# Kernel optimization log

Hardware: AMD Instinct MI355X
Metric: run time of the kernel (lower is better)

Reference implementation:

```python
import jax, jax.numpy as jnp
import numpy as np

N_HEADS = 16
D_EMBD = 1024
B, T = 2, 2048


def setup_inputs() -> dict:
    key = jax.random.key(0)
    k1, k2, k3 = jax.random.split(key, 3)
    x = jax.random.normal(k1, (B, T, D_EMBD), dtype=jnp.float32)
    W1 = jax.random.normal(k2, (D_EMBD, 3 * D_EMBD), dtype=jnp.float32) / np.sqrt(D_EMBD)
    b1 = jnp.zeros((3 * D_EMBD,), dtype=jnp.float32)
    W2 = jax.random.normal(k3, (D_EMBD, D_EMBD), dtype=jnp.float32) / np.sqrt(D_EMBD)
    b2 = jnp.zeros((D_EMBD,), dtype=jnp.float32)
    return {"x": x, "W1": W1, "b1": b1, "W2": W2, "b2": b2}


def reference(x, W1, b1, W2, b2):
    bs, t, d = x.shape
    h = N_HEADS
    kqv = x @ W1 + b1  # [b, t, 3d]
    # note original split order: k, q, v
    k, q, v = jnp.split(kqv, 3, axis=-1)
    # [b, t, d] -> [b, h, t, dh]
    def to_heads(z):
        return z.reshape(bs, t, h, d // h).transpose(0, 2, 1, 3)
    k, q, v = to_heads(k), to_heads(q), to_heads(v)
    mask = jnp.tril(jnp.ones((t, t), dtype=bool))
    attn = jnp.where(mask, jnp.einsum('bhqd,bhkd->bhqk', q, k), 0.0)  # softmax-free retention
    out = jnp.einsum('bhqk,bhkd->bhqd', attn, v)
    out = out.transpose(0, 2, 1, 3).reshape(bs, t, d)  # [b, t, d]
    return out @ W2 + b2
```

## Files before the change

kernel.cpp:

```cpp
#include <hip/hip_runtime.h>
#include <hip/hip_bf16.h>

typedef __bf16 bf16x8 __attribute__((ext_vector_type(8)));
typedef float f32x4 __attribute__((ext_vector_type(4)));
typedef float f32x16 __attribute__((ext_vector_type(16)));
typedef unsigned short ushort_t;
typedef unsigned short ushort8 __attribute__((ext_vector_type(8)));
typedef unsigned int uint4v __attribute__((ext_vector_type(4)));


__device__ inline void gload_lds16(const void* g, void* l) {
  __builtin_amdgcn_global_load_lds(
      (const __attribute__((address_space(1))) void*)g,
      (__attribute__((address_space(3))) void*)l, 16, 0, 0);
}

__device__ inline ushort_t f2bf(float f) {
  unsigned int u = __float_as_uint(f);
  unsigned int lsb = (u >> 16) & 1u;
  u += 0x7fffu + lsb;
  return (ushort_t)(u >> 16);
}


__global__ __launch_bounds__(256) void f32_to_bf16_vec(
    const float* __restrict__ in, ushort_t* __restrict__ out) {
  int i = (blockIdx.x * 256 + threadIdx.x) * 8;
  float4 a = *(const float4*)&in[i];
  float4 b = *(const float4*)&in[i + 4];
  ushort8 o;
  o[0] = f2bf(a.x); o[1] = f2bf(a.y); o[2] = f2bf(a.z); o[3] = f2bf(a.w);
  o[4] = f2bf(b.x); o[5] = f2bf(b.y); o[6] = f2bf(b.z); o[7] = f2bf(b.w);
  *(ushort8*)&out[i] = o;
}

__global__ __launch_bounds__(256) void transpose_f32_bf16(
    const float* __restrict__ in, ushort_t* __restrict__ out, int R, int C) {
  __shared__ float tile[32][33];
  const int tx = threadIdx.x & 31, ty = threadIdx.x >> 5;
  const int c0 = blockIdx.x * 32, r0 = blockIdx.y * 32;
#pragma unroll
  for (int i = 0; i < 32; i += 8)
    tile[ty + i][tx] = in[(size_t)(r0 + ty + i) * C + c0 + tx];
  __syncthreads();
#pragma unroll
  for (int i = 0; i < 32; i += 8)
    out[(size_t)(c0 + ty + i) * R + r0 + tx] = f2bf(tile[tx][ty + i]);
}

__global__ __launch_bounds__(256) void transpose_v(
    const ushort_t* __restrict__ kqv, ushort_t* __restrict__ vt) {
  __shared__ ushort_t tile[64 * 64];
  const int tt = blockIdx.x;
  const int bh = blockIdx.y;
  const int b = bh >> 4, h = bh & 15;
  const int tid = threadIdx.x;
#pragma unroll
  for (int p = 0; p < 2; p++) {
    const int tr = (tid >> 3) + p * 32;
    const int c8 = tid & 7;
    ushort8 v = *(const ushort8*)&kqv[(size_t)(b * 2048 + tt * 64 + tr) * 3072 +
                                      2048 + h * 64 + c8 * 8];
    *(ushort8*)&tile[tr * 64 + ((c8 ^ (tr & 7)) * 8)] = v;
  }
  __syncthreads();
  const int d = tid & 63;
#pragma unroll
  for (int p = 0; p < 2; p++) {
    const int t8 = (tid >> 6) + p * 4;
    ushort8 o;
#pragma unroll
    for (int j = 0; j < 8; j++) {
      const int t = t8 * 8 + j;
      o[j] = tile[t * 64 + (((d >> 3) ^ (t & 7)) * 8) + (d & 7)];
    }
    *(ushort8*)&vt[(size_t)(bh * 64 + d) * 2048 + tt * 64 + t8 * 8] = o;
  }
}


template <bool OUT_BF16>
__global__ __launch_bounds__(256) void gemm_bt(
    const ushort_t* __restrict__ A, const ushort_t* __restrict__ BT,
    const float* __restrict__ bias, void* __restrict__ Cout,
    int M, int N, int K) {
  __shared__ ushort_t lA[128 * 32];
  __shared__ ushort_t lB[128 * 32];
  const int tid = threadIdx.x;
  const int lane = tid & 63;
  const int wave = tid >> 6;
  const int wr = wave >> 1, wc = wave & 1;
  const int l16 = lane & 15, lhi = lane >> 4;
  const int bx = blockIdx.x, by = blockIdx.y;

  const ushort_t* gA = A + (size_t)(by * 128 + (tid >> 2)) * K + (tid & 3) * 8;
  const ushort_t* gB = BT + (size_t)(bx * 128 + (tid >> 2)) * K + (tid & 3) * 8;

  f32x4 acc[4][4] = {};

  for (int k0 = 0; k0 < K; k0 += 32) {
    gload_lds16(gA + k0, &lA[tid * 8]);
    gload_lds16(gA + k0 + (size_t)64 * K, &lA[tid * 8 + 2048]);
    gload_lds16(gB + k0, &lB[tid * 8]);
    gload_lds16(gB + k0 + (size_t)64 * K, &lB[tid * 8 + 2048]);
    __syncthreads();

    bf16x8 af[4], bfr[4];
#pragma unroll
    for (int m = 0; m < 4; m++)
      af[m] = *(const bf16x8*)&lA[(wr * 64 + m * 16 + l16) * 32 + lhi * 8];
#pragma unroll
    for (int n = 0; n < 4; n++)
      bfr[n] = *(const bf16x8*)&lB[(wc * 64 + n * 16 + l16) * 32 + lhi * 8];
#pragma unroll
    for (int m = 0; m < 4; m++)
#pragma unroll
      for (int n = 0; n < 4; n++)
        acc[m][n] = __builtin_amdgcn_mfma_f32_16x16x32_bf16(af[m], bfr[n],
                                                            acc[m][n], 0, 0, 0);
    __syncthreads();
  }

  const int r0 = by * 128 + wr * 64 + lhi * 4;
  const int c0 = bx * 128 + wc * 64 + l16;
#pragma unroll
  for (int m = 0; m < 4; m++)
#pragma unroll
    for (int n = 0; n < 4; n++) {
      const int col = c0 + n * 16;
      const float bv = bias[col];
#pragma unroll
      for (int j = 0; j < 4; j++) {
        const int row = r0 + m * 16 + j;
        const float v = acc[m][n][j] + bv;
        if (OUT_BF16)
          ((ushort_t*)Cout)[(size_t)row * N + col] = f2bf(v);
        else
          ((float*)Cout)[(size_t)row * N + col] = v;
      }
    }
}


__global__ __launch_bounds__(256) void attn_kernel(
    const ushort_t* __restrict__ kqv, const ushort_t* __restrict__ vt,
    ushort_t* __restrict__ ao) {
  __shared__ ushort_t lK[3][64 * 64];
  __shared__ ushort_t lVT[3][64 * 64];
  const int tid = threadIdx.x, lane = tid & 63, wave = tid >> 6;
  const int q_rel = lane & 31, hi = lane >> 5;
  const int L = blockIdx.x;
  const int W = (L & 7) * 64 + (L >> 3);
  const int qi = 15 - (W & 15);
  const int bh = W >> 4;
  const int b = bh >> 4, h = bh & 15;
  const int q0 = qi * 128;
  const ushort_t* base = kqv + (size_t)b * 2048 * 3072;
  const ushort_t* vbase = vt + (size_t)bh * 64 * 2048;

  size_t kg[2], vg[2];
  int ld[2];
#pragma unroll
  for (int p = 0; p < 2; p++) {
    const int slot = tid + p * 256;
    const int srow = slot >> 3;
    const int scb = (((slot & 7) * 16) ^ ((srow & 7) << 4)) >> 1;
    kg[p] = (size_t)srow * 3072 + h * 64 + scb;
    vg[p] = (size_t)srow * 2048 + scb;
    ld[p] = slot * 8;
  }

  const int wq0 = q0 + wave * 32;
  bf16x8 qf[4];
#pragma unroll
  for (int ds = 0; ds < 4; ds++)
    qf[ds] = *(const bf16x8*)&base[(size_t)(wq0 + q_rel) * 3072 + 1024 + h * 64 +
                                   ds * 16 + hi * 8];

  f32x16 oacc[2] = {};
  const int nkt = qi * 2 + 2;

#pragma unroll
  for (int p = 0; p < 2; p++) {
    gload_lds16(&base[kg[p]], &lK[0][ld[p]]);
    gload_lds16(&vbase[vg[p]], &lVT[0][ld[p]]);
  }
#pragma unroll
  for (int p = 0; p < 2; p++) {
    gload_lds16(&base[(size_t)64 * 3072 + kg[p]], &lK[1][ld[p]]);
    gload_lds16(&vbase[64 + vg[p]], &lVT[1][ld[p]]);
  }

  int cur = 0;
  for (int kt = 0; kt < nkt; ++kt) {
    if (kt + 1 < nkt) asm volatile("s_waitcnt vmcnt(4)" ::: "memory");
    else              asm volatile("s_waitcnt vmcnt(0)" ::: "memory");
    __builtin_amdgcn_s_barrier();
    asm volatile("" ::: "memory");

    if (kt + 2 < nkt) {
      const int pf = (cur + 2 >= 3) ? cur - 1 : cur + 2;
#pragma unroll
      for (int p = 0; p < 2; p++) {
        gload_lds16(&base[(size_t)(kt + 2) * 64 * 3072 + kg[p]], &lK[pf][ld[p]]);
        gload_lds16(&vbase[(size_t)(kt + 2) * 64 + vg[p]], &lVT[pf][ld[p]]);
      }
    }

    if (kt * 64 <= wq0 + 31) {
      const bool need_mask = (kt * 64 + 63) > wq0;
#pragma unroll
      for (int kb = 0; kb < 2; kb++) {
        f32x16 st = {};
        const int krow = kb * 32 + q_rel;
        const int ksw = krow & 7;
#pragma unroll
        for (int ds = 0; ds < 4; ds++) {
          bf16x8 kf = *(const bf16x8*)&lK[cur][krow * 64 + (((ds * 2 + hi) ^ ksw) * 8)];
          st = __builtin_amdgcn_mfma_f32_32x32x16_bf16(kf, qf[ds], st, 0, 0, 0);
        }
        if (need_mask) {
#pragma unroll
          for (int r = 0; r < 16; r++) {
            const int kgl = kt * 64 + kb * 32 + (r & 3) + 8 * (r >> 2) + 4 * hi;
            if (kgl > wq0 + q_rel) st[r] = 0.f;
          }
        }
        unsigned int w0, w1, w2, w3, w4, w5, w6, w7;
        {
          float e0 = st[0], e1 = st[1], e2 = st[2], e3 = st[3];
          float e4 = st[4], e5 = st[5], e6 = st[6], e7 = st[7];
          float e8 = st[8], e9 = st[9], e10 = st[10], e11 = st[11];
          float e12 = st[12], e13 = st[13], e14 = st[14], e15 = st[15];
          asm("v_cvt_pk_bf16_f32 %0, %1, %2" : "=v"(w0) : "v"(e0), "v"(e1));
          asm("v_cvt_pk_bf16_f32 %0, %1, %2" : "=v"(w1) : "v"(e2), "v"(e3));
          asm("v_cvt_pk_bf16_f32 %0, %1, %2" : "=v"(w2) : "v"(e4), "v"(e5));
          asm("v_cvt_pk_bf16_f32 %0, %1, %2" : "=v"(w3) : "v"(e6), "v"(e7));
          asm("v_cvt_pk_bf16_f32 %0, %1, %2" : "=v"(w4) : "v"(e8), "v"(e9));
          asm("v_cvt_pk_bf16_f32 %0, %1, %2" : "=v"(w5) : "v"(e10), "v"(e11));
          asm("v_cvt_pk_bf16_f32 %0, %1, %2" : "=v"(w6) : "v"(e12), "v"(e13));
          asm("v_cvt_pk_bf16_f32 %0, %1, %2" : "=v"(w7) : "v"(e14), "v"(e15));
        }
        asm("v_permlane32_swap_b32 %0, %1" : "+v"(w0), "+v"(w2));
        asm("v_permlane32_swap_b32 %0, %1" : "+v"(w1), "+v"(w3));
        asm("v_permlane32_swap_b32 %0, %1" : "+v"(w4), "+v"(w6));
        asm("v_permlane32_swap_b32 %0, %1" : "+v"(w5), "+v"(w7));
        uint4v u0 = {w0, w1, w2, w3};
        uint4v u1 = {w4, w5, w6, w7};
        bf16x8 pa0 = __builtin_bit_cast(bf16x8, u0);
        bf16x8 pa1 = __builtin_bit_cast(bf16x8, u1);
#pragma unroll
        for (int dt = 0; dt < 2; dt++) {
          const int vrow = dt * 32 + q_rel;
          const int vsw = vrow & 7;
          bf16x8 vf0 = *(const bf16x8*)&lVT[cur][vrow * 64 + (((kb * 4 + hi) ^ vsw) * 8)];
          bf16x8 vf1 = *(const bf16x8*)&lVT[cur][vrow * 64 + (((kb * 4 + 2 + hi) ^ vsw) * 8)];
          oacc[dt] = __builtin_amdgcn_mfma_f32_32x32x16_bf16(pa0, vf0, oacc[dt], 0, 0, 0);
          oacc[dt] = __builtin_amdgcn_mfma_f32_32x32x16_bf16(pa1, vf1, oacc[dt], 0, 0, 0);
        }
      }
    }

    cur = (cur + 1 >= 3) ? 0 : cur + 1;
  }

#pragma unroll
  for (int dt = 0; dt < 2; dt++)
#pragma unroll
    for (int r = 0; r < 16; r++) {
      const int q = (r & 3) + 8 * (r >> 2) + 4 * hi;
      const int row = wq0 + q;
      const int col = h * 64 + dt * 32 + q_rel;
      ao[(size_t)(b * 2048 + row) * 1024 + col] = f2bf(oacc[dt][r]);
    }
}


extern "C" void kernel_launch(void* const* d_in, const int* in_sizes, int n_in,
                              void* d_out, int out_size, void* d_ws, size_t ws_size,
                              hipStream_t stream) {
  const float* x  = (const float*)d_in[0];
  const float* W1 = (const float*)d_in[1];
  const float* b1 = (const float*)d_in[2];
  const float* W2 = (const float*)d_in[3];
  const float* b2 = (const float*)d_in[4];
  float* out = (float*)d_out;

  char* ws = (char*)d_ws;
  ushort_t* xb  = (ushort_t*)(ws);
  ushort_t* w1t = (ushort_t*)(ws + 8388608);
  ushort_t* w2t = (ushort_t*)(ws + 14680064);
  ushort_t* kqv = (ushort_t*)(ws + 16777216);
  ushort_t* ao  = (ushort_t*)(ws + 41943040);
  ushort_t* vtb = (ushort_t*)(ws);

  f32_to_bf16_vec<<<2048, 256, 0, stream>>>(x, xb);
  transpose_f32_bf16<<<dim3(96, 32), 256, 0, stream>>>(W1, w1t, 1024, 3072);
  transpose_f32_bf16<<<dim3(32, 32), 256, 0, stream>>>(W2, w2t, 1024, 1024);
  gemm_bt<true ><<<dim3(24, 32), 256, 0, stream>>>(xb, w1t, b1, kqv, 4096, 3072, 1024);
  transpose_v<<<dim3(32, 32), 256, 0, stream>>>(kqv, vtb);
  attn_kernel<<<dim3(512), 256, 0, stream>>>(kqv, vtb, ao);
  gemm_bt<false><<<dim3(8, 32), 256, 0, stream>>>(ao, w2t, b2, out, 4096, 1024, 1024);
}
```

Before: 209.7 us.

## Split attention KV tiles across waves with 64-row query blocks and LDS reduction

The attention kernel now uses 64-query blocks instead of 128, doubling the grid to 1024 workgroups. Each wave pair splits the two 32-key halves of every KV tile, and the partial outputs are summed through LDS at the end. The pipeline shrinks from triple to double buffering with a full vmcnt(0) wait per iteration, and the block-to-head mapping is reworked to group heads per XCD with staggered causal lengths. The aim is better load balance and occupancy for the causal workload, at the cost of less prefetch depth, an extra reduction pass, and K/V tiles loaded twice as often per query row.

```diff
diff --git a/kernel.cpp b/kernel.cpp
--- a/kernel.cpp
+++ b/kernel.cpp
@@ -145,16 +145,16 @@
 __global__ __launch_bounds__(256) void attn_kernel(
     const ushort_t* __restrict__ kqv, const ushort_t* __restrict__ vt,
     ushort_t* __restrict__ ao) {
-  __shared__ ushort_t lK[3][64 * 64];
-  __shared__ ushort_t lVT[3][64 * 64];
+  __shared__ ushort_t lK[2][64 * 64];
+  __shared__ ushort_t lVT[2][64 * 64];
   const int tid = threadIdx.x, lane = tid & 63, wave = tid >> 6;
   const int q_rel = lane & 31, hi = lane >> 5;
+  const int qs = wave & 1, kb = wave >> 1;
   const int L = blockIdx.x;
-  const int W = (L & 7) * 64 + (L >> 3);
-  const int qi = 15 - (W & 15);
-  const int bh = W >> 4;
+  const int xcd = L & 7, t = L >> 3;
+  const int bh = xcd * 4 + (t >> 5);
+  const int qj = 31 - ((t + bh * 7) & 31);
   const int b = bh >> 4, h = bh & 15;
-  const int q0 = qi * 128;
   const ushort_t* base = kqv + (size_t)b * 2048 * 3072;
   const ushort_t* vbase = vt + (size_t)bh * 64 * 2048;
 
@@ -170,7 +170,7 @@
     ld[p] = slot * 8;
   }
 
-  const int wq0 = q0 + wave * 32;
+  const int wq0 = qj * 64 + qs * 32;
   bf16x8 qf[4];
 #pragma unroll
   for (int ds = 0; ds < 4; ds++)
@@ -178,101 +178,104 @@
                                    ds * 16 + hi * 8];
 
   f32x16 oacc[2] = {};
-  const int nkt = qi * 2 + 2;
+  const int nkt = qj + 1;
 
 #pragma unroll
   for (int p = 0; p < 2; p++) {
     gload_lds16(&base[kg[p]], &lK[0][ld[p]]);
     gload_lds16(&vbase[vg[p]], &lVT[0][ld[p]]);
   }
-#pragma unroll
-  for (int p = 0; p < 2; p++) {
-    gload_lds16(&base[(size_t)64 * 3072 + kg[p]], &lK[1][ld[p]]);
-    gload_lds16(&vbase[64 + vg[p]], &lVT[1][ld[p]]);
-  }
 
   int cur = 0;
   for (int kt = 0; kt < nkt; ++kt) {
-    if (kt + 1 < nkt) asm volatile("s_waitcnt vmcnt(4)" ::: "memory");
-    else              asm volatile("s_waitcnt vmcnt(0)" ::: "memory");
+    asm volatile("s_waitcnt vmcnt(0)" ::: "memory");
     __builtin_amdgcn_s_barrier();
     asm volatile("" ::: "memory");
 
-    if (kt + 2 < nkt) {
-      const int pf = (cur + 2 >= 3) ? cur - 1 : cur + 2;
+    if (kt + 1 < nkt) {
 #pragma unroll
       for (int p = 0; p < 2; p++) {
-        gload_lds16(&base[(size_t)(kt + 2) * 64 * 3072 + kg[p]], &lK[pf][ld[p]]);
-        gload_lds16(&vbase[(size_t)(kt + 2) * 64 + vg[p]], &lVT[pf][ld[p]]);
+        gload_lds16(&base[(size_t)(kt + 1) * 64 * 3072 + kg[p]], &lK[cur ^ 1][ld[p]]);
+        gload_lds16(&vbase[(size_t)(kt + 1) * 64 + vg[p]], &lVT[cur ^ 1][ld[p]]);
       }
     }
 
-    if (kt * 64 <= wq0 + 31) {
-      const bool need_mask = (kt * 64 + 63) > wq0;
-#pragma unroll
-      for (int kb = 0; kb < 2; kb++) {
-        f32x16 st = {};
-        const int krow = kb * 32 + q_rel;
-        const int ksw = krow & 7;
-#pragma unroll
-        for (int ds = 0; ds < 4; ds++) {
-          bf16x8 kf = *(const bf16x8*)&lK[cur][krow * 64 + (((ds * 2 + hi) ^ ksw) * 8)];
-          st = __builtin_amdgcn_mfma_f32_32x32x16_bf16(kf, qf[ds], st, 0, 0, 0);
+    const int kv0 = kt * 64 + kb * 32;
+    if (kv0 <= wq0 + 31) {
+      f32x16 st = {};
+      const int krow = kb * 32 + q_rel;
+      const int ksw = krow & 7;
+#pragma unroll
+      for (int ds = 0; ds < 4; ds++) {
+        bf16x8 kf = *(const bf16x8*)&lK[cur][krow * 64 + (((ds * 2 + hi) ^ ksw) * 8)];
+        st = __builtin_amdgcn_mfma_f32_32x32x16_bf16(kf, qf[ds], st, 0, 0, 0);
+      }
+      if (kv0 + 31 > wq0) {
+#pragma unroll
+        for (int r = 0; r < 16; r++) {
+          const int kgl = kv0 + (r & 3) + 8 * (r >> 2) + 4 * hi;
+          if (kgl > wq0 + q_rel) st[r] = 0.f;
         }
-        if (need_mask) {
-#pragma unroll
-          for (int r = 0; r < 16; r++) {
-            const int kgl = kt * 64 + kb * 32 + (r & 3) + 8 * (r >> 2) + 4 * hi;
-            if (kgl > wq0 + q_rel) st[r] = 0.f;
-          }
-        }
-        unsigned int w0, w1, w2, w3, w4, w5, w6, w7;
-        {
-          float e0 = st[0], e1 = st[1], e2 = st[2], e3 = st[3];
-          float e4 = st[4], e5 = st[5], e6 = st[6], e7 = st[7];
-          float e8 = st[8], e9 = st[9], e10 = st[10], e11 = st[11];
-          float e12 = st[12], e13 = st[13], e14 = st[14], e15 = st[15];
-          asm("v_cvt_pk_bf16_f32 %0, %1, %2" : "=v"(w0) : "v"(e0), "v"(e1));
-          asm("v_cvt_pk_bf16_f32 %0, %1, %2" : "=v"(w1) : "v"(e2), "v"(e3));
-          asm("v_cvt_pk_bf16_f32 %0, %1, %2" : "=v"(w2) : "v"(e4), "v"(e5));
-          asm("v_cvt_pk_bf16_f32 %0, %1, %2" : "=v"(w3) : "v"(e6), "v"(e7));
-          asm("v_cvt_pk_bf16_f32 %0, %1, %2" : "=v"(w4) : "v"(e8), "v"(e9));
-          asm("v_cvt_pk_bf16_f32 %0, %1, %2" : "=v"(w5) : "v"(e10), "v"(e11));
-          asm("v_cvt_pk_bf16_f32 %0, %1, %2" : "=v"(w6) : "v"(e12), "v"(e13));
-          asm("v_cvt_pk_bf16_f32 %0, %1, %2" : "=v"(w7) : "v"(e14), "v"(e15));
-        }
-        asm("v_permlane32_swap_b32 %0, %1" : "+v"(w0), "+v"(w2));
-        asm("v_permlane32_swap_b32 %0, %1" : "+v"(w1), "+v"(w3));
-        asm("v_permlane32_swap_b32 %0, %1" : "+v"(w4), "+v"(w6));
-        asm("v_permlane32_swap_b32 %0, %1" : "+v"(w5), "+v"(w7));
-        uint4v u0 = {w0, w1, w2, w3};
-        uint4v u1 = {w4, w5, w6, w7};
-        bf16x8 pa0 = __builtin_bit_cast(bf16x8, u0);
-        bf16x8 pa1 = __builtin_bit_cast(bf16x8, u1);
-#pragma unroll
-        for (int dt = 0; dt < 2; dt++) {
-          const int vrow = dt * 32 + q_rel;
-          const int vsw = vrow & 7;
-          bf16x8 vf0 = *(const bf16x8*)&lVT[cur][vrow * 64 + (((kb * 4 + hi) ^ vsw) * 8)];
-          bf16x8 vf1 = *(const bf16x8*)&lVT[cur][vrow * 64 + (((kb * 4 + 2 + hi) ^ vsw) * 8)];
-          oacc[dt] = __builtin_amdgcn_mfma_f32_32x32x16_bf16(pa0, vf0, oacc[dt], 0, 0, 0);
-          oacc[dt] = __builtin_amdgcn_mfma_f32_32x32x16_bf16(pa1, vf1, oacc[dt], 0, 0, 0);
-        }
+      }
+      unsigned int w0, w1, w2, w3, w4, w5, w6, w7;
+      {
+        float e0 = st[0], e1 = st[1], e2 = st[2], e3 = st[3];
+        float e4 = st[4], e5 = st[5], e6 = st[6], e7 = st[7];
+        float e8 = st[8], e9 = st[9], e10 = st[10], e11 = st[11];
+        float e12 = st[12], e13 = st[13], e14 = st[14], e15 = st[15];
+        asm("v_cvt_pk_bf16_f32 %0, %1, %2" : "=v"(w0) : "v"(e0), "v"(e1));
+        asm("v_cvt_pk_bf16_f32 %0, %1, %2" : "=v"(w1) : "v"(e2), "v"(e3));
+        asm("v_cvt_pk_bf16_f32 %0, %1, %2" : "=v"(w2) : "v"(e4), "v"(e5));
+        asm("v_cvt_pk_bf16_f32 %0, %1, %2" : "=v"(w3) : "v"(e6), "v"(e7));
+        asm("v_cvt_pk_bf16_f32 %0, %1, %2" : "=v"(w4) : "v"(e8), "v"(e9));
+        asm("v_cvt_pk_bf16_f32 %0, %1, %2" : "=v"(w5) : "v"(e10), "v"(e11));
+        asm("v_cvt_pk_bf16_f32 %0, %1, %2" : "=v"(w6) : "v"(e12), "v"(e13));
+        asm("v_cvt_pk_bf16_f32 %0, %1, %2" : "=v"(w7) : "v"(e14), "v"(e15));
+      }
+      asm("v_permlane32_swap_b32 %0, %1" : "+v"(w0), "+v"(w2));
+      asm("v_permlane32_swap_b32 %0, %1" : "+v"(w1), "+v"(w3));
+      asm("v_permlane32_swap_b32 %0, %1" : "+v"(w4), "+v"(w6));
+      asm("v_permlane32_swap_b32 %0, %1" : "+v"(w5), "+v"(w7));
+      uint4v u0 = {w0, w1, w2, w3};
+      uint4v u1 = {w4, w5, w6, w7};
+      bf16x8 pa0 = __builtin_bit_cast(bf16x8, u0);
+      bf16x8 pa1 = __builtin_bit_cast(bf16x8, u1);
+#pragma unroll
+      for (int dt = 0; dt < 2; dt++) {
+        const int vrow = dt * 32 + q_rel;
+        const int vsw = vrow & 7;
+        bf16x8 vf0 = *(const bf16x8*)&lVT[cur][vrow * 64 + (((kb * 4 + hi) ^ vsw) * 8)];
+        bf16x8 vf1 = *(const bf16x8*)&lVT[cur][vrow * 64 + (((kb * 4 + 2 + hi) ^ vsw) * 8)];
+        oacc[dt] = __builtin_amdgcn_mfma_f32_32x32x16_bf16(pa0, vf0, oacc[dt], 0, 0, 0);
+        oacc[dt] = __builtin_amdgcn_mfma_f32_32x32x16_bf16(pa1, vf1, oacc[dt], 0, 0, 0);
       }
     }
 
-    cur = (cur + 1 >= 3) ? 0 : cur + 1;
-  }
-
-#pragma unroll
-  for (int dt = 0; dt < 2; dt++)
-#pragma unroll
-    for (int r = 0; r < 16; r++) {
-      const int q = (r & 3) + 8 * (r >> 2) + 4 * hi;
-      const int row = wq0 + q;
-      const int col = h * 64 + dt * 32 + q_rel;
-      ao[(size_t)(b * 2048 + row) * 1024 + col] = f2bf(oacc[dt][r]);
-    }
+    cur ^= 1;
+  }
+
+  __syncthreads();
+  float* red = (float*)&lK[0][0];
+  if (kb == 1) {
+#pragma unroll
+    for (int dt = 0; dt < 2; dt++)
+#pragma unroll
+      for (int r = 0; r < 16; r++)
+        red[qs * 2048 + (dt * 16 + r) * 64 + lane] = oacc[dt][r];
+  }
+  __syncthreads();
+  if (kb == 0) {
+#pragma unroll
+    for (int dt = 0; dt < 2; dt++)
+#pragma unroll
+      for (int r = 0; r < 16; r++) {
+        const float v = oacc[dt][r] + red[qs * 2048 + (dt * 16 + r) * 64 + lane];
+        const int q = (r & 3) + 8 * (r >> 2) + 4 * hi;
+        const int row = wq0 + q;
+        const int col = h * 64 + dt * 32 + q_rel;
+        ao[(size_t)(b * 2048 + row) * 1024 + col] = f2bf(v);
+      }
+  }
 }
 
 
@@ -299,6 +302,6 @@
   transpose_f32_bf16<<<dim3(32, 32), 256, 0, stream>>>(W2, w2t, 1024, 1024);
   gemm_bt<true ><<<dim3(24, 32), 256, 0, stream>>>(xb, w1t, b1, kqv, 4096, 3072, 1024);
   transpose_v<<<dim3(32, 32), 256, 0, stream>>>(kqv, vtb);
-  attn_kernel<<<dim3(512), 256, 0, stream>>>(kqv, vtb, ao);
+  attn_kernel<<<dim3(1024), 256, 0, stream>>>(kqv, vtb, ao);
   gemm_bt<false><<<dim3(8, 32), 256, 0, stream>>>(ao, w2t, b2, out, 4096, 1024, 1024);
 }
```

Result: faster. 199.2 us (-5.0%).
